# Optimization experiments

Measured on AMD Instinct MI355X. Metric: run time of the kernel, lower is better.

## Reference

```python
import jax, jax.numpy as jnp
import numpy as np

B, N, F_IN = 2, 2048, 256
HEADS, F_OUT = 8, 32
NEG_SLOPE = 0.01  # torch F.leaky_relu default


def setup_inputs() -> dict:
    key = jax.random.key(0)
    k1, k2, k3, k4 = jax.random.split(key, 4)
    stdv = 1.0 / np.sqrt(F_OUT * HEADS)
    h = jax.random.normal(k1, (B, N, F_IN), dtype=jnp.float32)
    adj = jax.random.uniform(k2, (B, N, N), dtype=jnp.float32)
    W = jax.random.normal(k3, (F_IN, F_OUT * HEADS), dtype=jnp.float32) * stdv
    a = jax.random.normal(k4, (2 * F_OUT, 1), dtype=jnp.float32) * stdv
    return {"h": h, "adj": adj, "W": W, "a": a}


def reference(h, adj, W, a):
    # adj is accepted by the original forward but never used (dense attention).
    b, n, _ = h.shape
    f = a.shape[0] // 2
    heads = W.shape[1] // f
    Wh = (h @ W).reshape(b, n, heads, f)            # [b,n,h,f]
    a1 = a[:f, 0]                                    # attends to source i
    a2 = a[f:, 0]                                    # attends to target j
    e1 = jnp.einsum('bnhf,f->bhn', Wh, a1)           # [b,h,n]
    e2 = jnp.einsum('bnhf,f->bhn', Wh, a2)           # [b,h,n]
    # e[b,h,i,j] = leaky_relu(a1.Wh_i + a2.Wh_j) == a^T [Wh_i || Wh_j]
    e = jax.nn.leaky_relu(e1[:, :, :, None] + e2[:, :, None, :], NEG_SLOPE)
    att = jax.nn.softmax(e, axis=-1)                 # softmax over neighbors j
    h_prime = jnp.einsum('bhij,bjhf->bihf', att, Wh)  # [b,n,h,f]
    return h_prime.reshape(b, n, heads * f)
```

## Files before the change

kernel.cpp:

```cpp
#include <hip/hip_runtime.h>
#include <math.h>

#define BATCH 2
#define NTOK  2048
#define FIN   256
#define HEADS 8
#define FOUT  32
#define BH    (BATCH*HEADS)
#define NCOL  (HEADS*FOUT)
#define ROWS  (BATCH*NTOK)

static const size_t OFF_E1   = 1048576;
static const size_t OFF_E2   = OFF_E1 + 32768;
static const size_t OFF_SKEY = OFF_E2 + 32768;
static const size_t OFF_SIDX = OFF_SKEY + 32768;
static const size_t OFF_W1S  = OFF_SIDX + 32768;
static const size_t OFF_W2S  = OFF_W1S + 32768;
static const size_t OFF_S1   = OFF_W2S + 32768;
static const size_t OFF_P2   = OFF_S1 + 32784;
static const size_t OFF_V1   = OFF_P2 + 32784;
static const size_t OFF_P2V  = OFF_V1 + 16u*2049u*32u;
static const size_t OFF_PART = OFF_V1;

__global__ __launch_bounds__(256) void k_gemm(const float* __restrict__ h,
                                              const float* __restrict__ W,
                                              float* __restrict__ Wh) {
    __shared__ alignas(16) float As[2][32][68];
    __shared__ alignas(16) float Bs[2][32][72];
    const int tid  = threadIdx.x;
    const int row0 = blockIdx.x * 64;
    const int col0 = blockIdx.y * 64;
    const int tx   = tid & 15;
    const int ty   = tid >> 4;
    const int ar   = tid >> 3;
    const int akq  = tid & 7;
    const int bkr  = tid >> 4;
    const int bcf  = tid & 15;
    const int colf = col0 >> 2;

    const float4* __restrict__ h4 = (const float4*)h;
    const float4* __restrict__ W4 = (const float4*)W;

    float4 a0 = h4[(size_t)(row0 + ar)      * 64 + akq];
    float4 a1 = h4[(size_t)(row0 + 32 + ar) * 64 + akq];
    float4 b0 = W4[(size_t)(bkr)      * 64 + colf + bcf];
    float4 b1 = W4[(size_t)(16 + bkr) * 64 + colf + bcf];

    float4 acc0 = make_float4(0.f,0.f,0.f,0.f);
    float4 acc1 = make_float4(0.f,0.f,0.f,0.f);
    float4 acc2 = make_float4(0.f,0.f,0.f,0.f);
    float4 acc3 = make_float4(0.f,0.f,0.f,0.f);

    for (int t = 0; t < FIN / 32; ++t) {
        const int cur = t & 1;
        As[cur][akq*4+0][ar]      = a0.x;
        As[cur][akq*4+1][ar]      = a0.y;
        As[cur][akq*4+2][ar]      = a0.z;
        As[cur][akq*4+3][ar]      = a0.w;
        As[cur][akq*4+0][32 + ar] = a1.x;
        As[cur][akq*4+1][32 + ar] = a1.y;
        As[cur][akq*4+2][32 + ar] = a1.z;
        As[cur][akq*4+3][32 + ar] = a1.w;
        *(float4*)&Bs[cur][bkr][bcf*4]      = b0;
        *(float4*)&Bs[cur][16 + bkr][bcf*4] = b1;
        __syncthreads();
        if (t + 1 < FIN / 32) {
            const int kc = (t + 1) * 32;
            a0 = h4[(size_t)(row0 + ar)      * 64 + (kc >> 2) + akq];
            a1 = h4[(size_t)(row0 + 32 + ar) * 64 + (kc >> 2) + akq];
            b0 = W4[(size_t)(kc + bkr)      * 64 + colf + bcf];
            b1 = W4[(size_t)(kc + 16 + bkr) * 64 + colf + bcf];
        }
        #pragma unroll
        for (int k = 0; k < 32; ++k) {
            float4 a4 = *(const float4*)&As[cur][k][ty*4];
            float4 b4 = *(const float4*)&Bs[cur][k][tx*4];
            acc0.x += a4.x*b4.x; acc0.y += a4.x*b4.y; acc0.z += a4.x*b4.z; acc0.w += a4.x*b4.w;
            acc1.x += a4.y*b4.x; acc1.y += a4.y*b4.y; acc1.z += a4.y*b4.z; acc1.w += a4.y*b4.w;
            acc2.x += a4.z*b4.x; acc2.y += a4.z*b4.y; acc2.z += a4.z*b4.z; acc2.w += a4.z*b4.w;
            acc3.x += a4.w*b4.x; acc3.y += a4.w*b4.y; acc3.z += a4.w*b4.z; acc3.w += a4.w*b4.w;
        }
    }
    const int orow = row0 + ty*4;
    *(float4*)(Wh + (size_t)(orow + 0) * NCOL + col0 + tx*4) = acc0;
    *(float4*)(Wh + (size_t)(orow + 1) * NCOL + col0 + tx*4) = acc1;
    *(float4*)(Wh + (size_t)(orow + 2) * NCOL + col0 + tx*4) = acc2;
    *(float4*)(Wh + (size_t)(orow + 3) * NCOL + col0 + tx*4) = acc3;
}

__global__ __launch_bounds__(256) void k_e12(const float* __restrict__ Wh,
                                             const float* __restrict__ a,
                                             float* __restrict__ e1,
                                             float* __restrict__ e2) {
    __shared__ float av[64];
    const int tid = threadIdx.x;
    if (tid < 64) av[tid] = a[tid];
    __syncthreads();

    const int g     = blockIdx.x * 256 + tid;
    const int n_lin = g >> 3;
    const int hh    = g & 7;
    const float4* p = (const float4*)(Wh + (size_t)n_lin * NCOL + hh * FOUT);
    float s1 = 0.f, s2 = 0.f;
    #pragma unroll
    for (int q = 0; q < 8; ++q) {
        float4 v = p[q];
        s1 += v.x * av[q*4+0] + v.y * av[q*4+1] + v.z * av[q*4+2] + v.w * av[q*4+3];
        s2 += v.x * av[32+q*4+0] + v.y * av[32+q*4+1] + v.z * av[32+q*4+2] + v.w * av[32+q*4+3];
    }
    const int b  = n_lin >> 11;
    const int n  = n_lin & (NTOK - 1);
    const int bh = b * HEADS + hh;
    e1[bh * NTOK + n] = s1;
    e2[bh * NTOK + n] = s2;
}

__device__ __forceinline__ unsigned long long sortkey(float f, int j) {
    unsigned int b = __float_as_uint(f);
    unsigned int u = (b & 0x80000000u) ? ~b : (b | 0x80000000u);
    return ((unsigned long long)u << 32) | (unsigned int)(NTOK - 1 - j);
}

__global__ __launch_bounds__(256) void k_rank8(const float* __restrict__ e2g,
                                               int* __restrict__ partial) {
    __shared__ alignas(16) unsigned long long ch[256];
    const int tid = threadIdx.x;
    const int bh  = blockIdx.x;
    const int jt  = blockIdx.y;
    const int kt  = blockIdx.z;
    const int kbase = kt * 256;
    ch[tid] = sortkey(e2g[bh * NTOK + kbase + tid], kbase + tid);
    __syncthreads();

    const int j = jt * 256 + tid;
    const unsigned long long my = sortkey(e2g[bh * NTOK + j], j);
    int rank = 0;
    const ulonglong2* c2 = (const ulonglong2*)ch;
    #pragma unroll 8
    for (int q = 0; q < 128; ++q) {
        ulonglong2 v = c2[q];
        rank += (v.x > my);
        rank += (v.y > my);
    }
    partial[(kt * BH + bh) * NTOK + j] = rank;
}

__global__ __launch_bounds__(256) void k_scatter(const float* __restrict__ e2g,
                                                 const int* __restrict__ partial,
                                                 float* __restrict__ skey,
                                                 int* __restrict__ sidx,
                                                 float* __restrict__ w1s,
                                                 float* __restrict__ w2s) {
    const int tid = threadIdx.x;
    const int bh  = blockIdx.x;
    const int jt  = blockIdx.y;
    const int j   = jt * 256 + tid;
    int rank = 0;
    #pragma unroll
    for (int kt = 0; kt < 8; ++kt)
        rank += partial[(kt * BH + bh) * NTOK + j];
    const float my = e2g[bh * NTOK + j];
    skey[bh * NTOK + rank] = my;
    sidx[bh * NTOK + rank] = j;
    w1s[bh * NTOK + rank]  = expf(my);
    w2s[bh * NTOK + rank]  = expf(0.01f * my);
}

__global__ __launch_bounds__(1024) void k_vscan(const float* __restrict__ Wh,
                                                const int* __restrict__ sidx,
                                                const float* __restrict__ w1s,
                                                const float* __restrict__ w2s,
                                                float* __restrict__ V1,
                                                float* __restrict__ P2V,
                                                float* __restrict__ S1,
                                                float* __restrict__ P2) {
    __shared__ float4 wtot[16];
    __shared__ float4 woff[16];
    const int t    = threadIdx.x;
    const int lane = t & 63;
    const int wv   = t >> 6;
    const int fg   = blockIdx.x;
    const int bh   = blockIdx.y;
    const int z    = blockIdx.z;
    const int b    = bh >> 3;
    const int hh   = bh & 7;
    const float* wsrc = z ? w2s : w1s;

    const int j0 = 2 * t;
    float4 v0, v1;
    if (fg < 8) {
        int sj0 = sidx[bh * NTOK + j0];
        int sj1 = sidx[bh * NTOK + j0 + 1];
        float w0 = wsrc[bh * NTOK + j0];
        float w1 = wsrc[bh * NTOK + j0 + 1];
        float4 g0 = *(const float4*)(Wh + (size_t)(b * NTOK + sj0) * NCOL + hh * FOUT + fg * 4);
        float4 g1 = *(const float4*)(Wh + (size_t)(b * NTOK + sj1) * NCOL + hh * FOUT + fg * 4);
        v0 = make_float4(w0 * g0.x, w0 * g0.y, w0 * g0.z, w0 * g0.w);
        v1 = make_float4(w1 * g1.x, w1 * g1.y, w1 * g1.z, w1 * g1.w);
    } else {
        v0 = make_float4(wsrc[bh * NTOK + j0],     0.f, 0.f, 0.f);
        v1 = make_float4(wsrc[bh * NTOK + j0 + 1], 0.f, 0.f, 0.f);
    }

    float4 s = make_float4(v0.x + v1.x, v0.y + v1.y, v0.z + v1.z, v0.w + v1.w);
    #pragma unroll
    for (int d = 1; d < 64; d <<= 1) {
        float ux = __shfl_up(s.x, (unsigned)d, 64);
        float uy = __shfl_up(s.y, (unsigned)d, 64);
        float uz = __shfl_up(s.z, (unsigned)d, 64);
        float uw = __shfl_up(s.w, (unsigned)d, 64);
        if (lane >= d) { s.x += ux; s.y += uy; s.z += uz; s.w += uw; }
    }
    float4 pair = make_float4(v0.x + v1.x, v0.y + v1.y, v0.z + v1.z, v0.w + v1.w);
    float4 excl = make_float4(s.x - pair.x, s.y - pair.y, s.z - pair.z, s.w - pair.w);
    if (lane == 63) wtot[wv] = s;
    __syncthreads();
    if (t < 16) {
        float4 ws = wtot[t];
        float4 inc = ws;
        #pragma unroll
        for (int d = 1; d < 16; d <<= 1) {
            float ux = __shfl_up(inc.x, (unsigned)d, 16);
            float uy = __shfl_up(inc.y, (unsigned)d, 16);
            float uz = __shfl_up(inc.z, (unsigned)d, 16);
            float uw = __shfl_up(inc.w, (unsigned)d, 16);
            if ((t & 15) >= d) { inc.x += ux; inc.y += uy; inc.z += uz; inc.w += uw; }
        }
        woff[t] = make_float4(inc.x - ws.x, inc.y - ws.y, inc.z - ws.z, inc.w - ws.w);
    }
    __syncthreads();

    float4 base = woff[wv];
    float4 i0 = make_float4(base.x + excl.x + v0.x, base.y + excl.y + v0.y,
                            base.z + excl.z + v0.z, base.w + excl.w + v0.w);
    float4 i1 = make_float4(i0.x + v1.x, i0.y + v1.y, i0.z + v1.z, i0.w + v1.w);

    if (fg < 8) {
        float* dst = z ? P2V : V1;
        float* plane = dst + ((size_t)bh * 8 + fg) * (2049u * 4u);
        *(float4*)(plane + (size_t)(j0 + 1) * 4) = i0;
        *(float4*)(plane + (size_t)(j0 + 2) * 4) = i1;
        if (t == 0)
            *(float4*)plane = make_float4(0.f,0.f,0.f,0.f);
    } else {
        float* dst = z ? P2 : S1;
        dst[bh * 2049 + j0 + 1] = i0.x;
        dst[bh * 2049 + j0 + 2] = i1.x;
        if (t == 0) dst[bh * 2049] = 0.f;
    }
}

__global__ __launch_bounds__(256) void k_out(const float* __restrict__ skey,
                                             const float* __restrict__ e1g,
                                             const float* __restrict__ S1,
                                             const float* __restrict__ P2,
                                             const float* __restrict__ V1,
                                             const float* __restrict__ P2V,
                                             float* __restrict__ out) {
    __shared__ float keys[NTOK];
    const int tid = threadIdx.x;
    const int it  = blockIdx.x;
    const int bh  = blockIdx.y;
    const int b   = bh >> 3;
    const int hh  = bh & 7;
    #pragma unroll
    for (int q = 0; q < 8; ++q)
        keys[q * 256 + tid] = skey[bh * NTOK + q * 256 + tid];
    __syncthreads();

    const int i  = it * 32 + (tid >> 3);
    const int fg = tid & 7;
    const float e1v = e1g[bh * NTOK + i];
    const float th  = -e1v;
    int lo = 0, hi = NTOK;
    while (lo < hi) {
        int mid = (lo + hi) >> 1;
        if (keys[mid] > th) lo = mid + 1; else hi = mid;
    }
    const int k = lo;
    const float A = expf(e1v);
    const float C = expf(0.01f * e1v);
    const float s1  = S1[bh * 2049 + k];
    const float p2k = P2[bh * 2049 + k];
    const float p2t = P2[bh * 2049 + 2048];
    const float l   = A * s1 + C * (p2t - p2k);
    const float inv = 1.0f / l;
    const float* v1p  = V1  + ((size_t)bh * 8 + fg) * (2049u * 4u);
    const float* p2vp = P2V + ((size_t)bh * 8 + fg) * (2049u * 4u);
    float4 v1   = *(const float4*)(v1p  + (size_t)k * 4);
    float4 p2v  = *(const float4*)(p2vp + (size_t)k * 4);
    float4 p2vt = *(const float4*)(p2vp + (size_t)2048 * 4);
    float4 o;
    o.x = (A * v1.x + C * (p2vt.x - p2v.x)) * inv;
    o.y = (A * v1.y + C * (p2vt.y - p2v.y)) * inv;
    o.z = (A * v1.z + C * (p2vt.z - p2v.z)) * inv;
    o.w = (A * v1.w + C * (p2vt.w - p2v.w)) * inv;
    *(float4*)(out + (size_t)(b * NTOK + i) * NCOL + hh * FOUT + fg * 4) = o;
}

extern "C" void kernel_launch(void* const* d_in, const int* in_sizes, int n_in,
                              void* d_out, int out_size, void* d_ws, size_t ws_size,
                              hipStream_t stream) {
    const float* h = (const float*)d_in[0];
    const float* W = (const float*)d_in[2];
    const float* a = (const float*)d_in[3];
    float* out = (float*)d_out;
    float* ws  = (float*)d_ws;

    float* Wh   = ws;
    float* e1   = ws + OFF_E1;
    float* e2   = ws + OFF_E2;
    float* skey = ws + OFF_SKEY;
    int*   sidx = (int*)(ws + OFF_SIDX);
    float* w1s  = ws + OFF_W1S;
    float* w2s  = ws + OFF_W2S;
    float* S1   = ws + OFF_S1;
    float* P2   = ws + OFF_P2;
    float* V1   = ws + OFF_V1;
    float* P2V  = ws + OFF_P2V;
    int*   part = (int*)(ws + OFF_PART);

    k_gemm   <<<dim3(ROWS / 64, NCOL / 64), 256, 0, stream>>>(h, W, Wh);
    k_e12    <<<dim3(ROWS * HEADS / 256),   256, 0, stream>>>(Wh, a, e1, e2);
    k_rank8  <<<dim3(BH, 8, 8),             256, 0, stream>>>(e2, part);
    k_scatter<<<dim3(BH, 8),                256, 0, stream>>>(e2, part, skey, sidx, w1s, w2s);
    k_vscan  <<<dim3(9, BH, 2),            1024, 0, stream>>>(Wh, sidx, w1s, w2s, V1, P2V, S1, P2);
    k_out    <<<dim3(NTOK / 32, BH),        256, 0, stream>>>(skey, e1, S1, P2, V1, P2V, out);
}
```

Baseline: 122.1 us.

## Use split-fp16 MFMA GEMM with fused e1/e2, merge rank and scatter kernels

Replaces the fp32 SIMT GEMM with a hi/lo fp16 split (3 MFMA products per tile) on matrix cores, preceded by a split/transpose kernel. The attention projections e1/e2 are computed in the GEMM epilogue with wave shuffles, which removes the separate k_e12 pass. The rank partial-count kernel and the scatter kernel are merged into one kernel that keeps all keys in LDS. This trades an extra conversion kernel and a small precision change for fewer launches and faster matrix math.

```diff
diff --git a/kernel.cpp b/kernel.cpp
--- a/kernel.cpp
+++ b/kernel.cpp
@@ -9,6 +9,10 @@
 #define BH    (BATCH*HEADS)
 #define NCOL  (HEADS*FOUT)
 #define ROWS  (BATCH*NTOK)
+
+typedef _Float16 f16;
+typedef _Float16 f16x8 __attribute__((ext_vector_type(8)));
+typedef float    f32x4 __attribute__((ext_vector_type(4)));
 
 static const size_t OFF_E1   = 1048576;
 static const size_t OFF_E2   = OFF_E1 + 32768;
@@ -20,99 +24,149 @@
 static const size_t OFF_P2   = OFF_S1 + 32784;
 static const size_t OFF_V1   = OFF_P2 + 32784;
 static const size_t OFF_P2V  = OFF_V1 + 16u*2049u*32u;
-static const size_t OFF_PART = OFF_V1;
-
-__global__ __launch_bounds__(256) void k_gemm(const float* __restrict__ h,
-                                              const float* __restrict__ W,
-                                              float* __restrict__ Wh) {
-    __shared__ alignas(16) float As[2][32][68];
-    __shared__ alignas(16) float Bs[2][32][72];
+static const size_t OFF_HHI  = OFF_P2V + 16u*2049u*32u;
+static const size_t OFF_HLO  = OFF_HHI + 524288;
+static const size_t OFF_WTHI = OFF_HLO + 524288;
+static const size_t OFF_WTLO = OFF_WTHI + 32768;
+
+__global__ __launch_bounds__(256) void k_split(const float* __restrict__ h,
+                                               const float* __restrict__ W,
+                                               f16* __restrict__ hhi, f16* __restrict__ hlo,
+                                               f16* __restrict__ wthi, f16* __restrict__ wtlo) {
+    const int tid = threadIdx.x;
+    if (blockIdx.x < 512) {
+        const size_t base = ((size_t)blockIdx.x * 256 + tid) * 8;
+        const float4 v0 = *(const float4*)(h + base);
+        const float4 v1 = *(const float4*)(h + base + 4);
+        const float xs[8] = {v0.x,v0.y,v0.z,v0.w,v1.x,v1.y,v1.z,v1.w};
+        f16x8 hi8, lo8;
+        #pragma unroll
+        for (int i = 0; i < 8; ++i) {
+            float xv = xs[i] * 16.0f;
+            f16 hv = (f16)xv;
+            hi8[i] = hv;
+            lo8[i] = (f16)(xv - (float)hv);
+        }
+        *(f16x8*)(hhi + base) = hi8;
+        *(f16x8*)(hlo + base) = lo8;
+    } else {
+        const int k0 = (blockIdx.x - 512) * 16;
+        const int c  = tid;
+        f16x8 hiA, loA, hiB, loB;
+        #pragma unroll
+        for (int j = 0; j < 8; ++j) {
+            float xv = W[(size_t)(k0 + j) * 256 + c] * 4096.0f;
+            f16 hv = (f16)xv;
+            hiA[j] = hv; loA[j] = (f16)(xv - (float)hv);
+        }
+        #pragma unroll
+        for (int j = 0; j < 8; ++j) {
+            float xv = W[(size_t)(k0 + 8 + j) * 256 + c] * 4096.0f;
+            f16 hv = (f16)xv;
+            hiB[j] = hv; loB[j] = (f16)(xv - (float)hv);
+        }
+        f16* pd = wthi + (size_t)c * 256 + k0;
+        f16* pe = wtlo + (size_t)c * 256 + k0;
+        *(f16x8*)pd = hiA; *(f16x8*)(pd + 8) = hiB;
+        *(f16x8*)pe = loA; *(f16x8*)(pe + 8) = loB;
+    }
+}
+
+__global__ __launch_bounds__(256) void k_mm(const f16* __restrict__ hhi, const f16* __restrict__ hlo,
+                                            const f16* __restrict__ wthi, const f16* __restrict__ wtlo,
+                                            const float* __restrict__ a,
+                                            float* __restrict__ Wh,
+                                            float* __restrict__ e1, float* __restrict__ e2) {
     const int tid  = threadIdx.x;
-    const int row0 = blockIdx.x * 64;
-    const int col0 = blockIdx.y * 64;
-    const int tx   = tid & 15;
-    const int ty   = tid >> 4;
-    const int ar   = tid >> 3;
-    const int akq  = tid & 7;
-    const int bkr  = tid >> 4;
-    const int bcf  = tid & 15;
-    const int colf = col0 >> 2;
-
-    const float4* __restrict__ h4 = (const float4*)h;
-    const float4* __restrict__ W4 = (const float4*)W;
-
-    float4 a0 = h4[(size_t)(row0 + ar)      * 64 + akq];
-    float4 a1 = h4[(size_t)(row0 + 32 + ar) * 64 + akq];
-    float4 b0 = W4[(size_t)(bkr)      * 64 + colf + bcf];
-    float4 b1 = W4[(size_t)(16 + bkr) * 64 + colf + bcf];
-
-    float4 acc0 = make_float4(0.f,0.f,0.f,0.f);
-    float4 acc1 = make_float4(0.f,0.f,0.f,0.f);
-    float4 acc2 = make_float4(0.f,0.f,0.f,0.f);
-    float4 acc3 = make_float4(0.f,0.f,0.f,0.f);
-
-    for (int t = 0; t < FIN / 32; ++t) {
-        const int cur = t & 1;
-        As[cur][akq*4+0][ar]      = a0.x;
-        As[cur][akq*4+1][ar]      = a0.y;
-        As[cur][akq*4+2][ar]      = a0.z;
-        As[cur][akq*4+3][ar]      = a0.w;
-        As[cur][akq*4+0][32 + ar] = a1.x;
-        As[cur][akq*4+1][32 + ar] = a1.y;
-        As[cur][akq*4+2][32 + ar] = a1.z;
-        As[cur][akq*4+3][32 + ar] = a1.w;
-        *(float4*)&Bs[cur][bkr][bcf*4]      = b0;
-        *(float4*)&Bs[cur][16 + bkr][bcf*4] = b1;
-        __syncthreads();
-        if (t + 1 < FIN / 32) {
-            const int kc = (t + 1) * 32;
-            a0 = h4[(size_t)(row0 + ar)      * 64 + (kc >> 2) + akq];
-            a1 = h4[(size_t)(row0 + 32 + ar) * 64 + (kc >> 2) + akq];
-            b0 = W4[(size_t)(kc + bkr)      * 64 + colf + bcf];
-            b1 = W4[(size_t)(kc + 16 + bkr) * 64 + colf + bcf];
-        }
-        #pragma unroll
-        for (int k = 0; k < 32; ++k) {
-            float4 a4 = *(const float4*)&As[cur][k][ty*4];
-            float4 b4 = *(const float4*)&Bs[cur][k][tx*4];
-            acc0.x += a4.x*b4.x; acc0.y += a4.x*b4.y; acc0.z += a4.x*b4.z; acc0.w += a4.x*b4.w;
-            acc1.x += a4.y*b4.x; acc1.y += a4.y*b4.y; acc1.z += a4.y*b4.z; acc1.w += a4.y*b4.w;
-            acc2.x += a4.z*b4.x; acc2.y += a4.z*b4.y; acc2.z += a4.z*b4.z; acc2.w += a4.z*b4.w;
-            acc3.x += a4.w*b4.x; acc3.y += a4.w*b4.y; acc3.z += a4.w*b4.z; acc3.w += a4.w*b4.w;
-        }
-    }
-    const int orow = row0 + ty*4;
-    *(float4*)(Wh + (size_t)(orow + 0) * NCOL + col0 + tx*4) = acc0;
-    *(float4*)(Wh + (size_t)(orow + 1) * NCOL + col0 + tx*4) = acc1;
-    *(float4*)(Wh + (size_t)(orow + 2) * NCOL + col0 + tx*4) = acc2;
-    *(float4*)(Wh + (size_t)(orow + 3) * NCOL + col0 + tx*4) = acc3;
-}
-
-__global__ __launch_bounds__(256) void k_e12(const float* __restrict__ Wh,
-                                             const float* __restrict__ a,
-                                             float* __restrict__ e1,
-                                             float* __restrict__ e2) {
-    __shared__ float av[64];
-    const int tid = threadIdx.x;
-    if (tid < 64) av[tid] = a[tid];
-    __syncthreads();
-
-    const int g     = blockIdx.x * 256 + tid;
-    const int n_lin = g >> 3;
-    const int hh    = g & 7;
-    const float4* p = (const float4*)(Wh + (size_t)n_lin * NCOL + hh * FOUT);
-    float s1 = 0.f, s2 = 0.f;
-    #pragma unroll
-    for (int q = 0; q < 8; ++q) {
-        float4 v = p[q];
-        s1 += v.x * av[q*4+0] + v.y * av[q*4+1] + v.z * av[q*4+2] + v.w * av[q*4+3];
-        s2 += v.x * av[32+q*4+0] + v.y * av[32+q*4+1] + v.z * av[32+q*4+2] + v.w * av[32+q*4+3];
-    }
-    const int b  = n_lin >> 11;
-    const int n  = n_lin & (NTOK - 1);
-    const int bh = b * HEADS + hh;
-    e1[bh * NTOK + n] = s1;
-    e2[bh * NTOK + n] = s2;
+    const int wv   = tid >> 6;
+    const int lane = tid & 63;
+    const int r    = lane & 15;
+    const int q    = lane >> 4;
+    const int row0 = blockIdx.x * 16;
+    const int col0 = wv * 64;
+    const int koff = q * 8;
+
+    const f16* pa_hi = hhi  + (size_t)(row0 + r) * 256 + koff;
+    const f16* pa_lo = hlo  + (size_t)(row0 + r) * 256 + koff;
+    const f16* pb_hi = wthi + (size_t)(col0 + r) * 256 + koff;
+    const f16* pb_lo = wtlo + (size_t)(col0 + r) * 256 + koff;
+
+    f32x4 acc[4];
+    #pragma unroll
+    for (int t = 0; t < 4; ++t) acc[t] = (f32x4){0.f,0.f,0.f,0.f};
+
+    struct FR { f16x8 ah, al, bh[4], bl[4]; };
+    auto ldfr = [&](int ch) {
+        FR f;
+        const int o = ch * 32;
+        f.ah = *(const f16x8*)(pa_hi + o);
+        f.al = *(const f16x8*)(pa_lo + o);
+        #pragma unroll
+        for (int t = 0; t < 4; ++t) {
+            f.bh[t] = *(const f16x8*)(pb_hi + t * (16 * 256) + o);
+            f.bl[t] = *(const f16x8*)(pb_lo + t * (16 * 256) + o);
+        }
+        return f;
+    };
+    auto dom = [&](const FR& f) {
+        #pragma unroll
+        for (int t = 0; t < 4; ++t) {
+            acc[t] = __builtin_amdgcn_mfma_f32_16x16x32_f16(f.ah, f.bh[t], acc[t], 0, 0, 0);
+            acc[t] = __builtin_amdgcn_mfma_f32_16x16x32_f16(f.ah, f.bl[t], acc[t], 0, 0, 0);
+            acc[t] = __builtin_amdgcn_mfma_f32_16x16x32_f16(f.al, f.bh[t], acc[t], 0, 0, 0);
+        }
+    };
+
+    FR fa = ldfr(0);
+    FR fb = ldfr(1);
+    #pragma unroll
+    for (int ch = 0; ch < 8; ch += 2) {
+        dom(fa);
+        if (ch + 2 < 8) fa = ldfr(ch + 2);
+        dom(fb);
+        if (ch + 3 < 8) fb = ldfr(ch + 3);
+    }
+
+    const float SC = 1.0f / 65536.0f;
+    #pragma unroll
+    for (int t = 0; t < 4; ++t) acc[t] *= SC;
+
+    #pragma unroll
+    for (int t = 0; t < 4; ++t)
+        #pragma unroll
+        for (int g = 0; g < 4; ++g)
+            Wh[(size_t)(row0 + q * 4 + g) * 256 + col0 + t * 16 + r] = acc[t][g];
+
+    const float av10 = a[r], av11 = a[16 + r], av20 = a[32 + r], av21 = a[48 + r];
+    float p1[8], p2[8];
+    #pragma unroll
+    for (int hp = 0; hp < 2; ++hp)
+        #pragma unroll
+        for (int g = 0; g < 4; ++g) {
+            p1[hp * 4 + g] = acc[2 * hp][g] * av10 + acc[2 * hp + 1][g] * av11;
+            p2[hp * 4 + g] = acc[2 * hp][g] * av20 + acc[2 * hp + 1][g] * av21;
+        }
+    #pragma unroll
+    for (int m = 1; m < 16; m <<= 1) {
+        #pragma unroll
+        for (int i = 0; i < 8; ++i) {
+            p1[i] += __shfl_xor(p1[i], m, 64);
+            p2[i] += __shfl_xor(p2[i], m, 64);
+        }
+    }
+    if (r == 0) {
+        #pragma unroll
+        for (int hp = 0; hp < 2; ++hp)
+            #pragma unroll
+            for (int g = 0; g < 4; ++g) {
+                const int row  = row0 + q * 4 + g;
+                const int b    = row >> 11;
+                const int n    = row & (NTOK - 1);
+                const int head = wv * 2 + hp;
+                e1[(b * HEADS + head) * NTOK + n] = p1[hp * 4 + g];
+                e2[(b * HEADS + head) * NTOK + n] = p2[hp * 4 + g];
+            }
+    }
 }
 
 __device__ __forceinline__ unsigned long long sortkey(float f, int j) {
@@ -121,49 +175,43 @@
     return ((unsigned long long)u << 32) | (unsigned int)(NTOK - 1 - j);
 }
 
-__global__ __launch_bounds__(256) void k_rank8(const float* __restrict__ e2g,
-                                               int* __restrict__ partial) {
-    __shared__ alignas(16) unsigned long long ch[256];
+__global__ __launch_bounds__(512) void k_rank(const float* __restrict__ e2g,
+                                              float* __restrict__ skey, int* __restrict__ sidx,
+                                              float* __restrict__ w1s, float* __restrict__ w2s) {
+    __shared__ unsigned long long keys[NTOK];
+    __shared__ int prank[2][256];
     const int tid = threadIdx.x;
     const int bh  = blockIdx.x;
     const int jt  = blockIdx.y;
-    const int kt  = blockIdx.z;
-    const int kbase = kt * 256;
-    ch[tid] = sortkey(e2g[bh * NTOK + kbase + tid], kbase + tid);
-    __syncthreads();
-
-    const int j = jt * 256 + tid;
-    const unsigned long long my = sortkey(e2g[bh * NTOK + j], j);
+    #pragma unroll
+    for (int qq = 0; qq < 4; ++qq) {
+        int idx = qq * 512 + tid;
+        keys[idx] = sortkey(e2g[bh * NTOK + idx], idx);
+    }
+    __syncthreads();
+    const int jl = tid & 255;
+    const int hf = tid >> 8;
+    const int j  = jt * 256 + jl;
+    const unsigned long long my = keys[j];
     int rank = 0;
-    const ulonglong2* c2 = (const ulonglong2*)ch;
+    const ulonglong2* c2 = (const ulonglong2*)(keys + hf * 1024);
     #pragma unroll 8
-    for (int q = 0; q < 128; ++q) {
-        ulonglong2 v = c2[q];
+    for (int qq = 0; qq < 512; ++qq) {
+        ulonglong2 v = c2[qq];
         rank += (v.x > my);
         rank += (v.y > my);
     }
-    partial[(kt * BH + bh) * NTOK + j] = rank;
-}
-
-__global__ __launch_bounds__(256) void k_scatter(const float* __restrict__ e2g,
-                                                 const int* __restrict__ partial,
-                                                 float* __restrict__ skey,
-                                                 int* __restrict__ sidx,
-                                                 float* __restrict__ w1s,
-                                                 float* __restrict__ w2s) {
-    const int tid = threadIdx.x;
-    const int bh  = blockIdx.x;
-    const int jt  = blockIdx.y;
-    const int j   = jt * 256 + tid;
-    int rank = 0;
-    #pragma unroll
-    for (int kt = 0; kt < 8; ++kt)
-        rank += partial[(kt * BH + bh) * NTOK + j];
-    const float my = e2g[bh * NTOK + j];
-    skey[bh * NTOK + rank] = my;
-    sidx[bh * NTOK + rank] = j;
-    w1s[bh * NTOK + rank]  = expf(my);
-    w2s[bh * NTOK + rank]  = expf(0.01f * my);
+    prank[hf][jl] = rank;
+    __syncthreads();
+    if (tid < 256) {
+        const int rk = prank[0][tid] + prank[1][tid];
+        const int jj = jt * 256 + tid;
+        const float myf = e2g[bh * NTOK + jj];
+        skey[bh * NTOK + rk] = myf;
+        sidx[bh * NTOK + rk] = jj;
+        w1s[bh * NTOK + rk]  = expf(myf);
+        w2s[bh * NTOK + rk]  = expf(0.01f * myf);
+    }
 }
 
 __global__ __launch_bounds__(1024) void k_vscan(const float* __restrict__ Wh,
@@ -318,12 +366,14 @@
     float* P2   = ws + OFF_P2;
     float* V1   = ws + OFF_V1;
     float* P2V  = ws + OFF_P2V;
-    int*   part = (int*)(ws + OFF_PART);
-
-    k_gemm   <<<dim3(ROWS / 64, NCOL / 64), 256, 0, stream>>>(h, W, Wh);
-    k_e12    <<<dim3(ROWS * HEADS / 256),   256, 0, stream>>>(Wh, a, e1, e2);
-    k_rank8  <<<dim3(BH, 8, 8),             256, 0, stream>>>(e2, part);
-    k_scatter<<<dim3(BH, 8),                256, 0, stream>>>(e2, part, skey, sidx, w1s, w2s);
-    k_vscan  <<<dim3(9, BH, 2),            1024, 0, stream>>>(Wh, sidx, w1s, w2s, V1, P2V, S1, P2);
-    k_out    <<<dim3(NTOK / 32, BH),        256, 0, stream>>>(skey, e1, S1, P2, V1, P2V, out);
-}
+    f16*   hhi  = (f16*)(ws + OFF_HHI);
+    f16*   hlo  = (f16*)(ws + OFF_HLO);
+    f16*   wthi = (f16*)(ws + OFF_WTHI);
+    f16*   wtlo = (f16*)(ws + OFF_WTLO);
+
+    k_split<<<528,            256, 0, stream>>>(h, W, hhi, hlo, wthi, wtlo);
+    k_mm   <<<256,            256, 0, stream>>>(hhi, hlo, wthi, wtlo, a, Wh, e1, e2);
+    k_rank <<<dim3(BH, 8),    512, 0, stream>>>(e2, skey, sidx, w1s, w2s);
+    k_vscan<<<dim3(9, BH, 2),1024, 0, stream>>>(Wh, sidx, w1s, w2s, V1, P2V, S1, P2);
+    k_out  <<<dim3(NTOK/32, BH), 256, 0, stream>>>(skey, e1, S1, P2, V1, P2V, out);
+}
```

Result: slower. 131.0 us (+7.3%).
